# Performance work log

Measured on AMD Instinct MI355X. Metric: run time of the kernel, lower is better.

## Reference

```python
import jax, jax.numpy as jnp
import numpy as np

TOPK_INC = 20  # top-k vertices per mention that form a hyperedge (torch.topk(attention_a, 20))
TOPK_OUT = 2   # top-k node reps concatenated into the output (torch.topk(X_score, k=2))


def _indicator_from_rows(att, idx):
    # att: [N, N], idx: [A] int. Rows with idx == 0 are skipped, as in the original loop.
    N = att.shape[0]
    rows = att[idx]                                   # [A, N] gather of attention rows
    _, top = jax.lax.top_k(rows, TOPK_INC)            # [A, TOPK_INC]
    mask = (idx != 0).astype(att.dtype)               # [A]
    vals = jnp.broadcast_to(mask[:, None], top.shape).reshape(-1)
    # scatter-max builds the 0/1 incidence vector (multiple mentions OR together)
    return jnp.zeros((N,), att.dtype).at[top.reshape(-1)].max(vals)  # [N]


def _forward_one(h, att, a_idx, b_idx, spk, W_w, W_b, S_w, S_b):
    # h: [N, H], att: [N, N], spk: [N] (single speaker row since speak_num == 1 -> E = 3)
    a_ind = _indicator_from_rows(att, a_idx)
    b_ind = _indicator_from_rows(att, b_idx)
    Hyper0 = jnp.stack([a_ind, b_ind, spk], axis=0)   # [E, N] binary incidence
    Dv = 1.0 / jnp.sqrt(Hyper0.sum(axis=0) + 1.0)     # sqrt(inverse(diag(Dv) + I)) diagonal, [N]
    De = 1.0 / jnp.sqrt(Hyper0.sum(axis=1))           # sqrt(inverse(diag(De))) diagonal, [E]
    Hyper = Hyper0 @ att                              # [E, N]  (dropout is identity in eval)
    Hyper_att = jax.nn.softmax(Hyper, axis=-1)        # F.softmax over last dim for 2D input
    Hyper_prime = Hyper_att @ h                       # [E, H]
    w = jax.nn.softmax(Hyper_prime @ W_w.T + W_b, axis=0)[:, 0]  # [E]
    # A = diag(Dv) @ Hyper0.T @ diag(w) @ diag(De) @ Hyper @ diag(Dv); X = A @ h.
    # Associate as M @ (K @ h) to avoid materializing the [N, N] matrix A.
    K = (w * De)[:, None] * Hyper * Dv[None, :]       # [E, N]
    M = Hyper0.T * Dv[:, None]                        # [N, E]
    X = M @ (K @ h)                                   # [N, H]
    score = (X @ S_w.T + S_b)[:, 0]                   # [N]
    _, top = jax.lax.top_k(score, TOPK_OUT)           # [2]
    return X[top].reshape(-1)                         # [2*H]


def setup_inputs() -> dict:
    key = jax.random.key(0)
    B, N, H, A = 32, 1024, 768, 8
    ks = jax.random.split(key, 8)
    inp = jax.random.normal(ks[0], (B, N, H), dtype=jnp.float32)
    word_att = jax.random.uniform(ks[1], (B, 1, N, N), dtype=jnp.float32)
    a_idx = jax.random.randint(ks[2], (B, A), 0, N)
    b_idx = jax.random.randint(ks[3], (B, A), 0, N)
    speak_num = jnp.ones((B, 1), dtype=jnp.int64 if jax.config.jax_enable_x64 else jnp.int32)
    speak_all = jax.random.randint(ks[4], (B, 3, N), 0, 2).astype(jnp.float32)
    W_w = jax.random.normal(ks[5], (1, H), dtype=jnp.float32) * (1.0 / np.sqrt(H))
    W_b = jnp.zeros((1,), dtype=jnp.float32)
    score_w = jax.random.normal(ks[6], (1, H), dtype=jnp.float32) * (1.0 / np.sqrt(H))
    score_b = jnp.zeros((1,), dtype=jnp.float32)
    return {"input": inp, "word_att": word_att, "a_idx": a_idx, "b_idx": b_idx,
            "speak_num": speak_num, "speak_all": speak_all,
            "W_w": W_w, "W_b": W_b, "score_w": score_w, "score_b": score_b}


def reference(input, word_att, a_idx, b_idx, speak_num, speak_all, W_w, W_b, score_w, score_b):
    # speak_num is all ones by construction -> exactly one speaker hyperedge per sample (E = 3)
    att = word_att[:, 0]           # [B, N, N]
    spk = speak_all[:, 0]          # [B, N]
    f = jax.vmap(_forward_one, in_axes=(0, 0, 0, 0, 0, None, None, None, None))
    return f(input, att, a_idx, b_idx, spk, W_w, W_b, score_w, score_b)  # [B, 2*H]
```

## Files before the change

kernel.cpp:

```cpp
#include <hip/hip_runtime.h>
#include <math.h>

#define B_ 32
#define N_ 1024
#define H_ 768
#define A_ 8
#define TOPK_ 20
#define CH2_ 16
#define CH4_ 16

__device__ __forceinline__ float wsum(float x) {
#pragma unroll
    for (int off = 32; off > 0; off >>= 1) x += __shfl_xor(x, off);
    return x;
}

__global__ __launch_bounds__(1024) void k1_ind(
    const float* __restrict__ att, const int* __restrict__ a_idx,
    const int* __restrict__ b_idx, const float* __restrict__ speak_all,
    float* __restrict__ aind, float* __restrict__ bind,
    float* __restrict__ Dv, float* __restrict__ De)
{
    const int b = blockIdx.x;
    const int tid = threadIdx.x;
    const int w = tid >> 6, lane = tid & 63;
    __shared__ float s_ind[2][N_];
    __shared__ float s_red[3][16];

    s_ind[0][tid] = 0.f;
    s_ind[1][tid] = 0.f;
    __syncthreads();

    const int which = w >> 3;
    const int r = w & 7;
    const int idx = which ? b_idx[b * A_ + r] : a_idx[b * A_ + r];
    if (idx != 0) {
        const float* row = att + ((size_t)b * N_ + idx) * N_;
        float v[16];
#pragma unroll
        for (int k = 0; k < 16; ++k) v[k] = row[(k << 6) + lane];
        float* dst = s_ind[which];
        for (int t = 0; t < TOPK_; ++t) {
            float bv = v[0]; int bk = 0;
#pragma unroll
            for (int k = 1; k < 16; ++k)
                if (v[k] > bv) { bv = v[k]; bk = k; }
            int bc = (bk << 6) + lane;
#pragma unroll
            for (int off = 32; off > 0; off >>= 1) {
                float ov = __shfl_xor(bv, off);
                int oc = __shfl_xor(bc, off);
                if (ov > bv || (ov == bv && oc < bc)) { bv = ov; bc = oc; }
            }
            if (lane == 0) dst[bc] = 1.f;
            if (lane == (bc & 63)) v[bc >> 6] = -INFINITY;
        }
    }
    __syncthreads();

    const float sa = s_ind[0][tid], sb = s_ind[1][tid];
    const float ss = speak_all[(size_t)b * 3 * N_ + tid];
    aind[b * N_ + tid] = sa;
    bind[b * N_ + tid] = sb;
    Dv[b * N_ + tid] = 1.f / sqrtf(sa + sb + ss + 1.f);

    float p[3] = {sa, sb, ss};
#pragma unroll
    for (int e = 0; e < 3; ++e) {
        float x = wsum(p[e]);
        if (lane == 0) s_red[e][w] = x;
    }
    __syncthreads();
    if (tid < 3) {
        float s = 0.f;
        for (int i = 0; i < 16; ++i) s += s_red[tid][i];
        De[b * 3 + tid] = 1.f / sqrtf(s);
    }
}

__global__ __launch_bounds__(256) void k2_part(
    const float* __restrict__ att, const float* __restrict__ aind,
    const float* __restrict__ bind, const float* __restrict__ speak_all,
    float* __restrict__ Hpart)
{
    const int b = blockIdx.y, c = blockIdx.x;
    const int n0 = c * 64;
    const int t = threadIdx.x;
    __shared__ float sw[3][64];
    __shared__ int rows[64];
    __shared__ int s_nr;

    if (t < 192) {
        const int e = t >> 6, r = t & 63, n = n0 + r;
        float v;
        if (e == 0)      v = aind[b * N_ + n];
        else if (e == 1) v = bind[b * N_ + n];
        else             v = speak_all[(size_t)b * 3 * N_ + n];
        sw[e][r] = v;
    }
    __syncthreads();
    if (t < 64) {
        const bool act = (sw[0][t] != 0.f) || (sw[1][t] != 0.f) || (sw[2][t] != 0.f);
        const unsigned long long m = __ballot(act);
        if (act) rows[__popcll(m & ((1ull << t) - 1ull))] = t;
        if (t == 0) s_nr = (int)__popcll(m);
    }
    __syncthreads();
    const int nr = s_nr;

    float a0x=0,a0y=0,a0z=0,a0w=0, a1x=0,a1y=0,a1z=0,a1w=0, a2x=0,a2y=0,a2z=0,a2w=0;
    const float* base = att + (size_t)b * N_ * N_ + (size_t)n0 * N_ + t * 4;
#pragma unroll 2
    for (int i = 0; i < nr; ++i) {
        const int r = rows[i];
        const float x0 = sw[0][r], x1 = sw[1][r], x2 = sw[2][r];
        const float4 v = *(const float4*)(base + (size_t)r * N_);
        a0x += x0*v.x; a0y += x0*v.y; a0z += x0*v.z; a0w += x0*v.w;
        a1x += x1*v.x; a1y += x1*v.y; a1z += x1*v.z; a1w += x1*v.w;
        a2x += x2*v.x; a2y += x2*v.y; a2z += x2*v.z; a2w += x2*v.w;
    }
    float* hp = Hpart + (size_t)(b * CH2_ + c) * 3 * N_ + t * 4;
    *(float4*)(hp)          = make_float4(a0x, a0y, a0z, a0w);
    *(float4*)(hp + N_)     = make_float4(a1x, a1y, a1z, a1w);
    *(float4*)(hp + 2 * N_) = make_float4(a2x, a2y, a2z, a2w);
}

__global__ __launch_bounds__(256) void k3_wgg(
    const float* __restrict__ Hpart, const float* __restrict__ Dv,
    float* __restrict__ wArr, float* __restrict__ ggArr)
{
    const int e = blockIdx.x, b = blockIdx.y;
    const int t = threadIdx.x;
    const int lane = t & 63, wv = t >> 6;
    __shared__ float sred[4];

    float4 acc = make_float4(0.f, 0.f, 0.f, 0.f);
    for (int c = 0; c < CH2_; ++c) {
        const float4 v = *(const float4*)(Hpart + ((size_t)(b * CH2_ + c) * 3 + e) * N_ + t * 4);
        acc.x += v.x; acc.y += v.y; acc.z += v.z; acc.w += v.w;
    }
    float m = fmaxf(fmaxf(acc.x, acc.y), fmaxf(acc.z, acc.w));
#pragma unroll
    for (int off = 32; off > 0; off >>= 1) m = fmaxf(m, __shfl_xor(m, off));
    if (lane == 0) sred[wv] = m;
    __syncthreads();
    m = fmaxf(fmaxf(sred[0], sred[1]), fmaxf(sred[2], sred[3]));
    __syncthreads();
    float z = __expf(acc.x - m) + __expf(acc.y - m) + __expf(acc.z - m) + __expf(acc.w - m);
    z = wsum(z);
    if (lane == 0) sred[wv] = z;
    __syncthreads();
    const float iZ = 1.f / (sred[0] + sred[1] + sred[2] + sred[3]);

    const float4 dv = *(const float4*)(Dv + b * N_ + t * 4);
    float4 w4 = make_float4(__expf(acc.x - m) * iZ, __expf(acc.y - m) * iZ,
                            __expf(acc.z - m) * iZ, __expf(acc.w - m) * iZ);
    float4 g4 = make_float4(acc.x * dv.x, acc.y * dv.y, acc.z * dv.z, acc.w * dv.w);
    *(float4*)(wArr  + ((size_t)(b * 3 + e)) * N_ + t * 4) = w4;
    *(float4*)(ggArr + ((size_t)(b * 3 + e)) * N_ + t * 4) = g4;
}

__global__ __launch_bounds__(192) void k4_part(
    const float* __restrict__ h, const float* __restrict__ wArr,
    const float* __restrict__ ggArr, float* __restrict__ UGpart)
{
    const int b = blockIdx.y, c = blockIdx.x;
    const int n0 = c * 64;
    const int t = threadIdx.x;
    __shared__ float sw[6][64];
    for (int i = t; i < 384; i += 192) {
        const int s = i >> 6, r = i & 63;
        sw[s][r] = (s < 3) ? wArr[((size_t)(b * 3 + s)) * N_ + n0 + r]
                           : ggArr[((size_t)(b * 3 + s - 3)) * N_ + n0 + r];
    }
    __syncthreads();

    float u0x=0,u0y=0,u0z=0,u0w=0, u1x=0,u1y=0,u1z=0,u1w=0, u2x=0,u2y=0,u2z=0,u2w=0;
    float g0x=0,g0y=0,g0z=0,g0w=0, g1x=0,g1y=0,g1z=0,g1w=0, g2x=0,g2y=0,g2z=0,g2w=0;
    const float* base = h + (size_t)b * N_ * H_ + (size_t)n0 * H_ + t * 4;
#pragma unroll 4
    for (int r = 0; r < 64; ++r) {
        const float4 v = *(const float4*)(base + (size_t)r * H_);
        const float w0 = sw[0][r], w1 = sw[1][r], w2 = sw[2][r];
        const float g0 = sw[3][r], g1 = sw[4][r], g2 = sw[5][r];
        u0x += w0*v.x; u0y += w0*v.y; u0z += w0*v.z; u0w += w0*v.w;
        u1x += w1*v.x; u1y += w1*v.y; u1z += w1*v.z; u1w += w1*v.w;
        u2x += w2*v.x; u2y += w2*v.y; u2z += w2*v.z; u2w += w2*v.w;
        g0x += g0*v.x; g0y += g0*v.y; g0z += g0*v.z; g0w += g0*v.w;
        g1x += g1*v.x; g1y += g1*v.y; g1z += g1*v.z; g1w += g1*v.w;
        g2x += g2*v.x; g2y += g2*v.y; g2z += g2*v.z; g2w += g2*v.w;
    }
    float* up = UGpart + (size_t)(b * CH4_ + c) * 6 * H_ + t * 4;
    *(float4*)(up)          = make_float4(u0x, u0y, u0z, u0w);
    *(float4*)(up + H_)     = make_float4(u1x, u1y, u1z, u1w);
    *(float4*)(up + 2*H_)   = make_float4(u2x, u2y, u2z, u2w);
    *(float4*)(up + 3*H_)   = make_float4(g0x, g0y, g0z, g0w);
    *(float4*)(up + 4*H_)   = make_float4(g1x, g1y, g1z, g1w);
    *(float4*)(up + 5*H_)   = make_float4(g2x, g2y, g2z, g2w);
}

__global__ __launch_bounds__(256) void k4b_red(
    const float* __restrict__ UGpart, float* __restrict__ U, float* __restrict__ G)
{
    const int gid = blockIdx.x * 256 + threadIdx.x;
    const int b = gid / 1152;
    const int rem = gid % 1152;
    const int s = rem / 192;
    const int col = (rem % 192) * 4;

    float4 acc = make_float4(0.f, 0.f, 0.f, 0.f);
    for (int c = 0; c < CH4_; ++c) {
        const float4 v = *(const float4*)(UGpart + (size_t)(b * CH4_ + c) * 6 * H_ + s * H_ + col);
        acc.x += v.x; acc.y += v.y; acc.z += v.z; acc.w += v.w;
    }
    if (s < 3) *(float4*)(U + ((size_t)(b * 3 + s)) * H_ + col) = acc;
    else       *(float4*)(G + ((size_t)(b * 3 + s - 3)) * H_ + col) = acc;
}

__global__ __launch_bounds__(256) void k5_fin(
    const float* __restrict__ U, const float* __restrict__ G,
    const float* __restrict__ De, const float* __restrict__ Dv,
    const float* __restrict__ aind, const float* __restrict__ bind,
    const float* __restrict__ speak_all,
    const float* __restrict__ W_w, const float* __restrict__ W_b,
    const float* __restrict__ S_w, const float* __restrict__ S_b,
    float* __restrict__ out)
{
    const int b = blockIdx.x, tid = threadIdx.x;
    const int lane = tid & 63, wv = tid >> 6;
    __shared__ float sKh[3 * H_];
    __shared__ float sscore[N_];
    __shared__ float sred[16];
    __shared__ int sidx[4];

    const float* Ub = U + (size_t)b * 3 * H_;
    const float* Gb = G + (size_t)b * 3 * H_;

    float p0 = 0.f, p1 = 0.f, p2 = 0.f;
    for (int j = tid; j < H_; j += 256) {
        const float ww = W_w[j];
        p0 += Ub[j] * ww; p1 += Ub[H_ + j] * ww; p2 += Ub[2 * H_ + j] * ww;
    }
    p0 = wsum(p0); p1 = wsum(p1); p2 = wsum(p2);
    if (lane == 0) { sred[wv * 3 + 0] = p0; sred[wv * 3 + 1] = p1; sred[wv * 3 + 2] = p2; }
    __syncthreads();
    const float wb = W_b[0];
    const float l0 = sred[0] + sred[3] + sred[6] + sred[9]  + wb;
    const float l1 = sred[1] + sred[4] + sred[7] + sred[10] + wb;
    const float l2 = sred[2] + sred[5] + sred[8] + sred[11] + wb;
    const float mx = fmaxf(l0, fmaxf(l1, l2));
    const float e0 = expf(l0 - mx), e1 = expf(l1 - mx), e2 = expf(l2 - mx);
    const float inv = 1.f / (e0 + e1 + e2);
    const float wd0 = e0 * inv * De[b * 3 + 0];
    const float wd1 = e1 * inv * De[b * 3 + 1];
    const float wd2 = e2 * inv * De[b * 3 + 2];

    for (int j = tid; j < H_; j += 256) {
        sKh[j]          = wd0 * Gb[j];
        sKh[H_ + j]     = wd1 * Gb[H_ + j];
        sKh[2 * H_ + j] = wd2 * Gb[2 * H_ + j];
    }
    __syncthreads();

    float q0 = 0.f, q1 = 0.f, q2 = 0.f;
    for (int j = tid; j < H_; j += 256) {
        const float sw2 = S_w[j];
        q0 += sKh[j] * sw2; q1 += sKh[H_ + j] * sw2; q2 += sKh[2 * H_ + j] * sw2;
    }
    q0 = wsum(q0); q1 = wsum(q1); q2 = wsum(q2);
    if (lane == 0) { sred[wv * 3 + 0] = q0; sred[wv * 3 + 1] = q1; sred[wv * 3 + 2] = q2; }
    __syncthreads();
    q0 = sred[0] + sred[3] + sred[6] + sred[9];
    q1 = sred[1] + sred[4] + sred[7] + sred[10];
    q2 = sred[2] + sred[5] + sred[8] + sred[11];

    const float sb0 = S_b[0];
    const float* av = aind + b * N_;
    const float* bv2 = bind + b * N_;
    const float* dv = Dv + b * N_;
    const float* sv = speak_all + (size_t)b * 3 * N_;
    for (int n = tid; n < N_; n += 256)
        sscore[n] = dv[n] * (av[n] * q0 + bv2[n] * q1 + sv[n] * q2) + sb0;
    __syncthreads();

    int r0;
    {
        float best = -INFINITY; int bi = N_;
        for (int n = tid; n < N_; n += 256) {
            const float s = sscore[n];
            if (s > best || (s == best && n < bi)) { best = s; bi = n; }
        }
#pragma unroll
        for (int off = 32; off > 0; off >>= 1) {
            const float ov = __shfl_xor(best, off); const int oi = __shfl_xor(bi, off);
            if (ov > best || (ov == best && oi < bi)) { best = ov; bi = oi; }
        }
        if (lane == 0) { sred[wv] = best; sidx[wv] = bi; }
        __syncthreads();
        float v = -INFINITY; int i = N_;
        for (int k = 0; k < 4; ++k)
            if (sred[k] > v || (sred[k] == v && sidx[k] < i)) { v = sred[k]; i = sidx[k]; }
        r0 = i;
    }
    __syncthreads();
    int r1;
    {
        float best = -INFINITY; int bi = N_;
        for (int n = tid; n < N_; n += 256) {
            if (n == r0) continue;
            const float s = sscore[n];
            if (s > best || (s == best && n < bi)) { best = s; bi = n; }
        }
#pragma unroll
        for (int off = 32; off > 0; off >>= 1) {
            const float ov = __shfl_xor(best, off); const int oi = __shfl_xor(bi, off);
            if (ov > best || (ov == best && oi < bi)) { best = ov; bi = oi; }
        }
        if (lane == 0) { sred[wv] = best; sidx[wv] = bi; }
        __syncthreads();
        float v = -INFINITY; int i = N_;
        for (int k = 0; k < 4; ++k)
            if (sred[k] > v || (sred[k] == v && sidx[k] < i)) { v = sred[k]; i = sidx[k]; }
        r1 = i;
    }

    float* ob = out + (size_t)b * 2 * H_;
    {
        const float d = dv[r0], wa = av[r0], wbn = bv2[r0], wsv = sv[r0];
        for (int j = tid; j < H_; j += 256)
            ob[j] = d * (wa * sKh[j] + wbn * sKh[H_ + j] + wsv * sKh[2 * H_ + j]);
    }
    {
        const float d = dv[r1], wa = av[r1], wbn = bv2[r1], wsv = sv[r1];
        for (int j = tid; j < H_; j += 256)
            ob[H_ + j] = d * (wa * sKh[j] + wbn * sKh[H_ + j] + wsv * sKh[2 * H_ + j]);
    }
}

extern "C" void kernel_launch(void* const* d_in, const int* in_sizes, int n_in,
                              void* d_out, int out_size, void* d_ws, size_t ws_size,
                              hipStream_t stream)
{
    const float* h         = (const float*)d_in[0];
    const float* att       = (const float*)d_in[1];
    const int*   a_idx     = (const int*)d_in[2];
    const int*   b_idx     = (const int*)d_in[3];
    const float* speak_all = (const float*)d_in[5];
    const float* W_w       = (const float*)d_in[6];
    const float* W_b       = (const float*)d_in[7];
    const float* S_w       = (const float*)d_in[8];
    const float* S_b       = (const float*)d_in[9];
    float* out = (float*)d_out;

    float* ws     = (float*)d_ws;
    float* aind   = ws;
    float* bind   = aind + B_ * N_;
    float* Dv     = bind + B_ * N_;
    float* De     = Dv + B_ * N_;
    float* Hpart  = De + 128;
    float* wArr   = Hpart + B_ * CH2_ * 3 * N_;
    float* ggArr  = wArr + B_ * 3 * N_;
    float* UGpart = ggArr + B_ * 3 * N_;
    float* U      = UGpart + B_ * CH4_ * 6 * H_;
    float* G      = U + B_ * 3 * H_;

    k1_ind<<<B_, 1024, 0, stream>>>(att, a_idx, b_idx, speak_all, aind, bind, Dv, De);
    k2_part<<<dim3(CH2_, B_), 256, 0, stream>>>(att, aind, bind, speak_all, Hpart);
    k3_wgg<<<dim3(3, B_), 256, 0, stream>>>(Hpart, Dv, wArr, ggArr);
    k4_part<<<dim3(CH4_, B_), 192, 0, stream>>>(h, wArr, ggArr, UGpart);
    k4b_red<<<144, 256, 0, stream>>>(UGpart, U, G);
    k5_fin<<<B_, 256, 0, stream>>>(U, G, De, Dv, aind, bind, speak_all, W_w, W_b, S_w, S_b, out);
}
```

Baseline: 81.49 us.

## Double chunk count, replace partial-sum reduction kernel with atomics

```diff
diff --git a/kernel.cpp b/kernel.cpp
--- a/kernel.cpp
+++ b/kernel.cpp
@@ -6,8 +6,8 @@
 #define H_ 768
 #define A_ 8
 #define TOPK_ 20
-#define CH2_ 16
-#define CH4_ 16
+#define CH2_ 32
+#define CH4_ 32
 
 __device__ __forceinline__ float wsum(float x) {
 #pragma unroll
@@ -19,13 +19,19 @@
     const float* __restrict__ att, const int* __restrict__ a_idx,
     const int* __restrict__ b_idx, const float* __restrict__ speak_all,
     float* __restrict__ aind, float* __restrict__ bind,
-    float* __restrict__ Dv, float* __restrict__ De)
+    float* __restrict__ Dv, float* __restrict__ De,
+    float* __restrict__ U, float* __restrict__ G)
 {
     const int b = blockIdx.x;
     const int tid = threadIdx.x;
     const int w = tid >> 6, lane = tid & 63;
     __shared__ float s_ind[2][N_];
     __shared__ float s_red[3][16];
+
+    for (int i = tid; i < 3 * H_; i += 1024) {
+        U[(size_t)b * 3 * H_ + i] = 0.f;
+        G[(size_t)b * 3 * H_ + i] = 0.f;
+    }
 
     s_ind[0][tid] = 0.f;
     s_ind[1][tid] = 0.f;
@@ -84,14 +90,14 @@
     float* __restrict__ Hpart)
 {
     const int b = blockIdx.y, c = blockIdx.x;
-    const int n0 = c * 64;
+    const int n0 = c * 32;
     const int t = threadIdx.x;
-    __shared__ float sw[3][64];
-    __shared__ int rows[64];
+    __shared__ float sw[3][32];
+    __shared__ int rows[32];
     __shared__ int s_nr;
 
-    if (t < 192) {
-        const int e = t >> 6, r = t & 63, n = n0 + r;
+    if (t < 96) {
+        const int e = t >> 5, r = t & 31, n = n0 + r;
         float v;
         if (e == 0)      v = aind[b * N_ + n];
         else if (e == 1) v = bind[b * N_ + n];
@@ -100,7 +106,7 @@
     }
     __syncthreads();
     if (t < 64) {
-        const bool act = (sw[0][t] != 0.f) || (sw[1][t] != 0.f) || (sw[2][t] != 0.f);
+        const bool act = (t < 32) && (sw[0][t] != 0.f || sw[1][t] != 0.f || sw[2][t] != 0.f);
         const unsigned long long m = __ballot(act);
         if (act) rows[__popcll(m & ((1ull << t) - 1ull))] = t;
         if (t == 0) s_nr = (int)__popcll(m);
@@ -110,8 +116,39 @@
 
     float a0x=0,a0y=0,a0z=0,a0w=0, a1x=0,a1y=0,a1z=0,a1w=0, a2x=0,a2y=0,a2z=0,a2w=0;
     const float* base = att + (size_t)b * N_ * N_ + (size_t)n0 * N_ + t * 4;
-#pragma unroll 2
-    for (int i = 0; i < nr; ++i) {
+    int i = 0;
+    for (; i + 4 <= nr; i += 4) {
+        const int r0 = rows[i], r1 = rows[i+1], r2 = rows[i+2], r3 = rows[i+3];
+        const float4 v0 = *(const float4*)(base + (size_t)r0 * N_);
+        const float4 v1 = *(const float4*)(base + (size_t)r1 * N_);
+        const float4 v2 = *(const float4*)(base + (size_t)r2 * N_);
+        const float4 v3 = *(const float4*)(base + (size_t)r3 * N_);
+        {
+            const float x0 = sw[0][r0], x1 = sw[1][r0], x2 = sw[2][r0];
+            a0x += x0*v0.x; a0y += x0*v0.y; a0z += x0*v0.z; a0w += x0*v0.w;
+            a1x += x1*v0.x; a1y += x1*v0.y; a1z += x1*v0.z; a1w += x1*v0.w;
+            a2x += x2*v0.x; a2y += x2*v0.y; a2z += x2*v0.z; a2w += x2*v0.w;
+        }
+        {
+            const float x0 = sw[0][r1], x1 = sw[1][r1], x2 = sw[2][r1];
+            a0x += x0*v1.x; a0y += x0*v1.y; a0z += x0*v1.z; a0w += x0*v1.w;
+            a1x += x1*v1.x; a1y += x1*v1.y; a1z += x1*v1.z; a1w += x1*v1.w;
+            a2x += x2*v1.x; a2y += x2*v1.y; a2z += x2*v1.z; a2w += x2*v1.w;
+        }
+        {
+            const float x0 = sw[0][r2], x1 = sw[1][r2], x2 = sw[2][r2];
+            a0x += x0*v2.x; a0y += x0*v2.y; a0z += x0*v2.z; a0w += x0*v2.w;
+            a1x += x1*v2.x; a1y += x1*v2.y; a1z += x1*v2.z; a1w += x1*v2.w;
+            a2x += x2*v2.x; a2y += x2*v2.y; a2z += x2*v2.z; a2w += x2*v2.w;
+        }
+        {
+            const float x0 = sw[0][r3], x1 = sw[1][r3], x2 = sw[2][r3];
+            a0x += x0*v3.x; a0y += x0*v3.y; a0z += x0*v3.z; a0w += x0*v3.w;
+            a1x += x1*v3.x; a1y += x1*v3.y; a1z += x1*v3.z; a1w += x1*v3.w;
+            a2x += x2*v3.x; a2y += x2*v3.y; a2z += x2*v3.z; a2w += x2*v3.w;
+        }
+    }
+    for (; i < nr; ++i) {
         const int r = rows[i];
         const float x0 = sw[0][r], x1 = sw[1][r], x2 = sw[2][r];
         const float4 v = *(const float4*)(base + (size_t)r * N_);
@@ -119,6 +156,7 @@
         a1x += x1*v.x; a1y += x1*v.y; a1z += x1*v.z; a1w += x1*v.w;
         a2x += x2*v.x; a2y += x2*v.y; a2z += x2*v.z; a2w += x2*v.w;
     }
+
     float* hp = Hpart + (size_t)(b * CH2_ + c) * 3 * N_ + t * 4;
     *(float4*)(hp)          = make_float4(a0x, a0y, a0z, a0w);
     *(float4*)(hp + N_)     = make_float4(a1x, a1y, a1z, a1w);
@@ -146,15 +184,15 @@
     __syncthreads();
     m = fmaxf(fmaxf(sred[0], sred[1]), fmaxf(sred[2], sred[3]));
     __syncthreads();
-    float z = __expf(acc.x - m) + __expf(acc.y - m) + __expf(acc.z - m) + __expf(acc.w - m);
+    float z = expf(acc.x - m) + expf(acc.y - m) + expf(acc.z - m) + expf(acc.w - m);
     z = wsum(z);
     if (lane == 0) sred[wv] = z;
     __syncthreads();
     const float iZ = 1.f / (sred[0] + sred[1] + sred[2] + sred[3]);
 
     const float4 dv = *(const float4*)(Dv + b * N_ + t * 4);
-    float4 w4 = make_float4(__expf(acc.x - m) * iZ, __expf(acc.y - m) * iZ,
-                            __expf(acc.z - m) * iZ, __expf(acc.w - m) * iZ);
+    float4 w4 = make_float4(expf(acc.x - m) * iZ, expf(acc.y - m) * iZ,
+                            expf(acc.z - m) * iZ, expf(acc.w - m) * iZ);
     float4 g4 = make_float4(acc.x * dv.x, acc.y * dv.y, acc.z * dv.z, acc.w * dv.w);
     *(float4*)(wArr  + ((size_t)(b * 3 + e)) * N_ + t * 4) = w4;
     *(float4*)(ggArr + ((size_t)(b * 3 + e)) * N_ + t * 4) = g4;
@@ -162,14 +200,14 @@
 
 __global__ __launch_bounds__(192) void k4_part(
     const float* __restrict__ h, const float* __restrict__ wArr,
-    const float* __restrict__ ggArr, float* __restrict__ UGpart)
+    const float* __restrict__ ggArr, float* __restrict__ U, float* __restrict__ G)
 {
     const int b = blockIdx.y, c = blockIdx.x;
-    const int n0 = c * 64;
+    const int n0 = c * 32;
     const int t = threadIdx.x;
-    __shared__ float sw[6][64];
-    for (int i = t; i < 384; i += 192) {
-        const int s = i >> 6, r = i & 63;
+    __shared__ float sw[6][32];
+    if (t < 192) {
+        const int s = t >> 5, r = t & 31;
         sw[s][r] = (s < 3) ? wArr[((size_t)(b * 3 + s)) * N_ + n0 + r]
                            : ggArr[((size_t)(b * 3 + s - 3)) * N_ + n0 + r];
     }
@@ -179,7 +217,7 @@
     float g0x=0,g0y=0,g0z=0,g0w=0, g1x=0,g1y=0,g1z=0,g1w=0, g2x=0,g2y=0,g2z=0,g2w=0;
     const float* base = h + (size_t)b * N_ * H_ + (size_t)n0 * H_ + t * 4;
 #pragma unroll 4
-    for (int r = 0; r < 64; ++r) {
+    for (int r = 0; r < 32; ++r) {
         const float4 v = *(const float4*)(base + (size_t)r * H_);
         const float w0 = sw[0][r], w1 = sw[1][r], w2 = sw[2][r];
         const float g0 = sw[3][r], g1 = sw[4][r], g2 = sw[5][r];
@@ -190,31 +228,15 @@
         g1x += g1*v.x; g1y += g1*v.y; g1z += g1*v.z; g1w += g1*v.w;
         g2x += g2*v.x; g2y += g2*v.y; g2z += g2*v.z; g2w += g2*v.w;
     }
-    float* up = UGpart + (size_t)(b * CH4_ + c) * 6 * H_ + t * 4;
-    *(float4*)(up)          = make_float4(u0x, u0y, u0z, u0w);
-    *(float4*)(up + H_)     = make_float4(u1x, u1y, u1z, u1w);
-    *(float4*)(up + 2*H_)   = make_float4(u2x, u2y, u2z, u2w);
-    *(float4*)(up + 3*H_)   = make_float4(g0x, g0y, g0z, g0w);
-    *(float4*)(up + 4*H_)   = make_float4(g1x, g1y, g1z, g1w);
-    *(float4*)(up + 5*H_)   = make_float4(g2x, g2y, g2z, g2w);
-}
-
-__global__ __launch_bounds__(256) void k4b_red(
-    const float* __restrict__ UGpart, float* __restrict__ U, float* __restrict__ G)
-{
-    const int gid = blockIdx.x * 256 + threadIdx.x;
-    const int b = gid / 1152;
-    const int rem = gid % 1152;
-    const int s = rem / 192;
-    const int col = (rem % 192) * 4;
-
-    float4 acc = make_float4(0.f, 0.f, 0.f, 0.f);
-    for (int c = 0; c < CH4_; ++c) {
-        const float4 v = *(const float4*)(UGpart + (size_t)(b * CH4_ + c) * 6 * H_ + s * H_ + col);
-        acc.x += v.x; acc.y += v.y; acc.z += v.z; acc.w += v.w;
-    }
-    if (s < 3) *(float4*)(U + ((size_t)(b * 3 + s)) * H_ + col) = acc;
-    else       *(float4*)(G + ((size_t)(b * 3 + s - 3)) * H_ + col) = acc;
+
+    float* Ub = U + (size_t)b * 3 * H_ + t * 4;
+    float* Gb = G + (size_t)b * 3 * H_ + t * 4;
+    atomicAdd(Ub + 0, u0x); atomicAdd(Ub + 1, u0y); atomicAdd(Ub + 2, u0z); atomicAdd(Ub + 3, u0w);
+    atomicAdd(Ub + H_ + 0, u1x); atomicAdd(Ub + H_ + 1, u1y); atomicAdd(Ub + H_ + 2, u1z); atomicAdd(Ub + H_ + 3, u1w);
+    atomicAdd(Ub + 2*H_ + 0, u2x); atomicAdd(Ub + 2*H_ + 1, u2y); atomicAdd(Ub + 2*H_ + 2, u2z); atomicAdd(Ub + 2*H_ + 3, u2w);
+    atomicAdd(Gb + 0, g0x); atomicAdd(Gb + 1, g0y); atomicAdd(Gb + 2, g0z); atomicAdd(Gb + 3, g0w);
+    atomicAdd(Gb + H_ + 0, g1x); atomicAdd(Gb + H_ + 1, g1y); atomicAdd(Gb + H_ + 2, g1z); atomicAdd(Gb + H_ + 3, g1w);
+    atomicAdd(Gb + 2*H_ + 0, g2x); atomicAdd(Gb + 2*H_ + 1, g2y); atomicAdd(Gb + 2*H_ + 2, g2z); atomicAdd(Gb + 2*H_ + 3, g2w);
 }
 
 __global__ __launch_bounds__(256) void k5_fin(
@@ -360,14 +382,12 @@
     float* Hpart  = De + 128;
     float* wArr   = Hpart + B_ * CH2_ * 3 * N_;
     float* ggArr  = wArr + B_ * 3 * N_;
-    float* UGpart = ggArr + B_ * 3 * N_;
-    float* U      = UGpart + B_ * CH4_ * 6 * H_;
+    float* U      = ggArr + B_ * 3 * N_;
     float* G      = U + B_ * 3 * H_;
 
-    k1_ind<<<B_, 1024, 0, stream>>>(att, a_idx, b_idx, speak_all, aind, bind, Dv, De);
+    k1_ind<<<B_, 1024, 0, stream>>>(att, a_idx, b_idx, speak_all, aind, bind, Dv, De, U, G);
     k2_part<<<dim3(CH2_, B_), 256, 0, stream>>>(att, aind, bind, speak_all, Hpart);
     k3_wgg<<<dim3(3, B_), 256, 0, stream>>>(Hpart, Dv, wArr, ggArr);
-    k4_part<<<dim3(CH4_, B_), 192, 0, stream>>>(h, wArr, ggArr, UGpart);
-    k4b_red<<<144, 256, 0, stream>>>(UGpart, U, G);
+    k4_part<<<dim3(CH4_, B_), 192, 0, stream>>>(h, wArr, ggArr, U, G);
     k5_fin<<<B_, 256, 0, stream>>>(U, G, De, Dv, aind, bind, speak_all, W_w, W_b, S_w, S_b, out);
 }
```

After: 141.8 us. 1.74x slower.
